# Performance work log

Measured on AMD Instinct MI355X. Metric: run time of the kernel, lower is better.

Reference implementation:

```python
import jax, jax.numpy as jnp
import numpy as np

N, E = 50000, 1600000
C_IN, C_H, C_OUT = 36, 64, 64
EPS = 1e-16  # PyG softmax denominator epsilon


def setup_inputs() -> dict:
    key = jax.random.key(0)
    ks = jax.random.split(key, 48)
    inp = {}
    inp["features"] = jax.random.normal(ks[0], (N, C_IN), dtype=jnp.float32)
    inp["edge_attr"] = jax.random.uniform(ks[1], (E, 1), dtype=jnp.float32)
    inp["edge_index"] = jax.random.randint(ks[2], (2, E), 0, N, dtype=jnp.int32)
    dims = [(C_IN, C_H), (C_H, C_H), (C_H, C_H), (C_H, C_OUT)]
    i = 3
    for l, (din, dout) in enumerate(dims, 1):
        s = 1.0 / np.sqrt(din)
        inp[f"Wl{l}"] = jax.random.normal(ks[i], (din, dout), jnp.float32) * s; i += 1
        inp[f"bl{l}"] = jax.random.normal(ks[i], (dout,), jnp.float32) * 0.02; i += 1
        inp[f"Wr{l}"] = jax.random.normal(ks[i], (din, dout), jnp.float32) * s; i += 1
        inp[f"br{l}"] = jax.random.normal(ks[i], (dout,), jnp.float32) * 0.02; i += 1
        inp[f"We{l}"] = jax.random.normal(ks[i], (1, dout), jnp.float32); i += 1
        inp[f"att{l}"] = jax.random.normal(ks[i], (dout,), jnp.float32) * s; i += 1
        inp[f"bo{l}"] = jax.random.normal(ks[i], (dout,), jnp.float32) * 0.02; i += 1
    mlp = [(C_OUT, C_OUT // 2, "m1"), (C_OUT // 2, C_OUT // 4, "m2"), (C_OUT // 4, 1, "m3")]
    for din, dout, tag in mlp:
        s = 1.0 / np.sqrt(din)
        inp[f"W{tag}"] = jax.random.normal(ks[i], (din, dout), jnp.float32) * s; i += 1
        inp[f"b{tag}"] = jax.random.normal(ks[i], (dout,), jnp.float32) * 0.02; i += 1
    return inp


def gatv2_conv(x, src, dst, edge_attr, Wl, bl, Wr, br, We, att, bo):
    """Single-head GATv2Conv with edge features (PyG semantics)."""
    xl = x @ Wl + bl                      # [N, dout] source transform
    xr = x @ Wr + br                      # [N, dout] target transform
    ea = edge_attr @ We                   # [E, dout]
    e = jax.nn.leaky_relu(xl[src] + xr[dst] + ea, 0.2)  # [E, dout]
    score = e @ att                       # [E]
    # segment softmax over edges sharing a destination node
    m = jax.ops.segment_max(score, dst, num_segments=N)
    a = jnp.exp(score - m[dst])
    denom = jax.ops.segment_sum(a, dst, num_segments=N)
    alpha = a / (denom[dst] + EPS)
    out = jax.ops.segment_sum(xl[src] * alpha[:, None], dst, num_segments=N)
    return out + bo


def reference(features, edge_attr, edge_index,
              Wl1, bl1, Wr1, br1, We1, att1, bo1,
              Wl2, bl2, Wr2, br2, We2, att2, bo2,
              Wl3, bl3, Wr3, br3, We3, att3, bo3,
              Wl4, bl4, Wr4, br4, We4, att4, bo4,
              Wm1, bm1, Wm2, bm2, Wm3, bm3):
    src, dst = edge_index[0], edge_index[1]
    x = jax.nn.relu(gatv2_conv(features, src, dst, edge_attr, Wl1, bl1, Wr1, br1, We1, att1, bo1))
    x = jax.nn.relu(gatv2_conv(x, src, dst, edge_attr, Wl2, bl2, Wr2, br2, We2, att2, bo2))
    x = jax.nn.relu(gatv2_conv(x, src, dst, edge_attr, Wl3, bl3, Wr3, br3, We3, att3, bo3))
    x = jax.nn.relu(gatv2_conv(x, src, dst, edge_attr, Wl4, bl4, Wr4, br4, We4, att4, bo4))
    x = jnp.mean(x, axis=-2)              # graph readout -> [C_OUT]
    x = jax.nn.relu(x @ Wm1 + bm1)
    x = jax.nn.relu(x @ Wm2 + bm2)
    return x @ Wm3 + bm3                  # [1]
```

## Files before the change

kernel.cpp:

```cpp
#include <hip/hip_runtime.h>


__device__ __forceinline__ int rfl(int v) { return __builtin_amdgcn_readfirstlane(v); }

#define NBK_MAX 256
#define BCAP 10240

__global__ void __launch_bounds__(256) k_scatter(
    const int* __restrict__ src, const int* __restrict__ dst,
    const float* __restrict__ ea_in,
    int* __restrict__ bcur, uint2* __restrict__ tmp, int E, int nbk) {
  __shared__ int cnt[NBK_MAX];
  __shared__ int cur[NBK_MAX];
  __shared__ int gbase[NBK_MAX];
  int tid = threadIdx.x;
  if (tid < nbk) { cnt[tid] = 0; cur[tid] = 0; }
  __syncthreads();
  int base = blockIdx.x * 4096 + tid;
  uint2 rec[16];
  #pragma unroll
  for (int k = 0; k < 16; k++) {
    int e = base + k * 256;
    if (e < E) {
      unsigned d = (unsigned)dst[e];
      rec[k] = make_uint2((d << 16) | (unsigned)src[e],
                          (unsigned)__float_as_int(ea_in[e]));
      atomicAdd(&cnt[d >> 8], 1);
    } else {
      rec[k] = make_uint2(0u, 0u);
    }
  }
  __syncthreads();
  if (tid < nbk) {
    int c = cnt[tid];
    gbase[tid] = (c > 0) ? atomicAdd(&bcur[tid * 16], c) : 0;
  }
  __syncthreads();
  #pragma unroll
  for (int k = 0; k < 16; k++) {
    int e = base + k * 256;
    if (e < E) {
      int b = (int)(rec[k].x >> 24);
      int slot = atomicAdd(&cur[b], 1);
      tmp[(size_t)b * BCAP + gbase[b] + slot] = rec[k];
    }
  }
}

__global__ void k_bscan(const int* __restrict__ bcur, int* __restrict__ boffs,
                        int nbk, int E) {
  __shared__ int wsum[4];
  int tid = threadIdx.x, lane = tid & 63, wv = tid >> 6;
  int v = (tid < nbk) ? bcur[tid * 16] : 0;
  int x = v;
  #pragma unroll
  for (int o = 1; o < 64; o <<= 1) {
    int t = __shfl_up(x, o, 64);
    if (lane >= o) x += t;
  }
  if (lane == 63) wsum[wv] = x;
  __syncthreads();
  int wo = 0;
  for (int k = 0; k < 4; k++) if (k < wv) wo += wsum[k];
  if (tid < nbk) boffs[tid] = wo + (x - v);
  if (tid == 0) boffs[nbk] = E;
}

__global__ void __launch_bounds__(256) k_csr(const int* __restrict__ bcur,
                                             const int* __restrict__ boffs,
                                             const uint2* __restrict__ tmp,
                                             int2* __restrict__ pairs,
                                             int* __restrict__ rowptr, int N) {
  __shared__ int cnt[256];
  __shared__ int pref[256];
  __shared__ int cur[256];
  __shared__ int wsum[4];
  int b = blockIdx.x;
  int n0 = b << 8;
  int tid = threadIdx.x, lane = tid & 63, wv = tid >> 6;
  cnt[tid] = 0;
  cur[tid] = 0;
  __syncthreads();
  int cb = bcur[b * 16];
  const uint2* tb = tmp + (size_t)b * BCAP;
  int lo = boffs[b];
  for (int k = tid; k < cb; k += 256)
    atomicAdd(&cnt[(int)(tb[k].x >> 16) - n0], 1);
  __syncthreads();
  int v = cnt[tid];
  int x = v;
  #pragma unroll
  for (int o = 1; o < 64; o <<= 1) {
    int t = __shfl_up(x, o, 64);
    if (lane >= o) x += t;
  }
  if (lane == 63) wsum[wv] = x;
  __syncthreads();
  int wo = 0;
  for (int k = 0; k < 4; k++) if (k < wv) wo += wsum[k];
  int start = lo + wo + (x - v);
  pref[tid] = start;
  int nn = n0 + tid;
  if (nn <= N) rowptr[nn] = start;
  __syncthreads();
  for (int k = tid; k < cb; k += 256) {
    uint2 rec = tb[k];
    int local = (int)(rec.x >> 16) - n0;
    int pos = pref[local] + atomicAdd(&cur[local], 1);
    pairs[pos] = make_int2((int)(rec.x & 0xffffu), (int)rec.y);
  }
}

template <int DIN>
__global__ void __launch_bounds__(256) k_transform(
    const float* __restrict__ x, const float* __restrict__ Wl, const float* __restrict__ bl,
    const float* __restrict__ Wr, const float* __restrict__ br,
    float* __restrict__ xl, float* __restrict__ xr, int nNodes) {
  __shared__ __align__(16) float sWl[DIN * 64];
  __shared__ __align__(16) float sWr[DIN * 64];
  __shared__ float sx[64][DIN + 1];
  int tid = threadIdx.x;
  for (int i = tid; i < DIN * 64; i += 256) { sWl[i] = Wl[i]; sWr[i] = Wr[i]; }
  int nb = blockIdx.x * 64;
  for (int i = tid; i < 64 * DIN; i += 256) {
    int ln = i / DIN, c = i % DIN;
    int g = nb + ln;
    sx[ln][c] = (g < nNodes) ? x[(size_t)g * DIN + c] : 0.f;
  }
  __syncthreads();
  int c4 = (tid & 15) * 4;
  int ns = (tid >> 4) * 4;
  float4 bl4 = *(const float4*)(bl + c4);
  float4 br4 = *(const float4*)(br + c4);
  float4 L0 = bl4, L1 = bl4, L2 = bl4, L3 = bl4;
  float4 R0 = br4, R1 = br4, R2 = br4, R3 = br4;
  const float* x0 = sx[ns + 0];
  const float* x1 = sx[ns + 1];
  const float* x2 = sx[ns + 2];
  const float* x3 = sx[ns + 3];
  #pragma unroll 4
  for (int k = 0; k < DIN; k++) {
    float4 wl = *(const float4*)(sWl + k * 64 + c4);
    float4 wr = *(const float4*)(sWr + k * 64 + c4);
    float a = x0[k], bb = x1[k], c = x2[k], dd = x3[k];
    L0.x = fmaf(a, wl.x, L0.x);  L0.y = fmaf(a, wl.y, L0.y);
    L0.z = fmaf(a, wl.z, L0.z);  L0.w = fmaf(a, wl.w, L0.w);
    R0.x = fmaf(a, wr.x, R0.x);  R0.y = fmaf(a, wr.y, R0.y);
    R0.z = fmaf(a, wr.z, R0.z);  R0.w = fmaf(a, wr.w, R0.w);
    L1.x = fmaf(bb, wl.x, L1.x); L1.y = fmaf(bb, wl.y, L1.y);
    L1.z = fmaf(bb, wl.z, L1.z); L1.w = fmaf(bb, wl.w, L1.w);
    R1.x = fmaf(bb, wr.x, R1.x); R1.y = fmaf(bb, wr.y, R1.y);
    R1.z = fmaf(bb, wr.z, R1.z); R1.w = fmaf(bb, wr.w, R1.w);
    L2.x = fmaf(c, wl.x, L2.x);  L2.y = fmaf(c, wl.y, L2.y);
    L2.z = fmaf(c, wl.z, L2.z);  L2.w = fmaf(c, wl.w, L2.w);
    R2.x = fmaf(c, wr.x, R2.x);  R2.y = fmaf(c, wr.y, R2.y);
    R2.z = fmaf(c, wr.z, R2.z);  R2.w = fmaf(c, wr.w, R2.w);
    L3.x = fmaf(dd, wl.x, L3.x); L3.y = fmaf(dd, wl.y, L3.y);
    L3.z = fmaf(dd, wl.z, L3.z); L3.w = fmaf(dd, wl.w, L3.w);
    R3.x = fmaf(dd, wr.x, R3.x); R3.y = fmaf(dd, wr.y, R3.y);
    R3.z = fmaf(dd, wr.z, R3.z); R3.w = fmaf(dd, wr.w, R3.w);
  }
  int g = nb + ns;
  if (g + 0 < nNodes) { *(float4*)(xl + (size_t)(g+0)*64 + c4) = L0; *(float4*)(xr + (size_t)(g+0)*64 + c4) = R0; }
  if (g + 1 < nNodes) { *(float4*)(xl + (size_t)(g+1)*64 + c4) = L1; *(float4*)(xr + (size_t)(g+1)*64 + c4) = R1; }
  if (g + 2 < nNodes) { *(float4*)(xl + (size_t)(g+2)*64 + c4) = L2; *(float4*)(xr + (size_t)(g+2)*64 + c4) = R2; }
  if (g + 3 < nNodes) { *(float4*)(xl + (size_t)(g+3)*64 + c4) = L3; *(float4*)(xr + (size_t)(g+3)*64 + c4) = R3; }
}

#define SC1(T, EA, OUT) { float u, acc; \
  u = T.x + fmaf(EA, We4.x, xr4.x); u = fmaxf(u, 0.2f * u); acc = at4.x * u; \
  u = T.y + fmaf(EA, We4.y, xr4.y); u = fmaxf(u, 0.2f * u); acc = fmaf(at4.y, u, acc); \
  u = T.z + fmaf(EA, We4.z, xr4.z); u = fmaxf(u, 0.2f * u); acc = fmaf(at4.z, u, acc); \
  u = T.w + fmaf(EA, We4.w, xr4.w); u = fmaxf(u, 0.2f * u); acc = fmaf(at4.w, u, acc); \
  OUT = acc; }

__global__ void __launch_bounds__(256, 5) k_edge(
    const float* __restrict__ xl, const float* __restrict__ xr,
    const int* __restrict__ rowptr, const int2* __restrict__ pairs,
    const float* __restrict__ We, const float* __restrict__ att,
    const float* __restrict__ bo, float* __restrict__ xout, int nNodes) {
  int lane = threadIdx.x & 63;
  int wv = rfl((int)(threadIdx.x >> 6));
  int n = rfl(blockIdx.x * 4 + wv);
  if (n >= nNodes) return;
  int c4 = lane & 15;
  int r  = lane >> 4;
  int cb = c4 * 4;

  float4 We4 = *(const float4*)(We + cb);
  float4 at4 = *(const float4*)(att + cb);
  float4 xr4 = *(const float4*)(xr + (size_t)n * 64 + cb);
  int s0 = rfl(rowptr[n]);
  int s1 = rfl(rowptr[n + 1]);
  int last = s1 - 1;

  float m = -3.0e38f, d = 0.f;
  float4 A = {0.f, 0.f, 0.f, 0.f};

  for (int kb = s0; kb < s1; kb += 16) {
    int cnt = rfl(min(16, s1 - kb));
    int2 p0 = pairs[min(kb + r,      last)];
    int2 p1 = pairs[min(kb + 4 + r,  last)];
    int2 p2 = pairs[min(kb + 8 + r,  last)];
    int2 p3 = pairs[min(kb + 12 + r, last)];
    float ea0 = __int_as_float(p0.y);
    float ea1 = __int_as_float(p1.y);
    float ea2 = __int_as_float(p2.y);
    float ea3 = __int_as_float(p3.y);

    float4 t0 = *(const float4*)(xl + (size_t)(unsigned)p0.x * 64 + cb);
    float4 t1 = *(const float4*)(xl + (size_t)(unsigned)p1.x * 64 + cb);
    float4 t2 = *(const float4*)(xl + (size_t)(unsigned)p2.x * 64 + cb);
    float4 t3 = *(const float4*)(xl + (size_t)(unsigned)p3.x * 64 + cb);

    float sc0, sc1, sc2, sc3;
    SC1(t0, ea0, sc0)
    SC1(t1, ea1, sc1)
    SC1(t2, ea2, sc2)
    SC1(t3, ea3, sc3)

    #pragma unroll
    for (int o = 1; o <= 8; o <<= 1) {
      sc0 += __shfl_xor(sc0, o, 64);
      sc1 += __shfl_xor(sc1, o, 64);
      sc2 += __shfl_xor(sc2, o, 64);
      sc3 += __shfl_xor(sc3, o, 64);
    }
    sc0 = (r < cnt)      ? sc0 : -3.0e38f;
    sc1 = (4 + r < cnt)  ? sc1 : -3.0e38f;
    sc2 = (8 + r < cnt)  ? sc2 : -3.0e38f;
    sc3 = (12 + r < cnt) ? sc3 : -3.0e38f;

    float mc = fmaxf(fmaxf(sc0, sc1), fmaxf(sc2, sc3));
    mc = fmaxf(mc, __shfl_xor(mc, 16, 64));
    mc = fmaxf(mc, __shfl_xor(mc, 32, 64));
    float newm = fmaxf(m, mc);
    float rf = __expf(m - newm);
    float a0 = __expf(sc0 - newm);
    float a1 = __expf(sc1 - newm);
    float a2 = __expf(sc2 - newm);
    float a3 = __expf(sc3 - newm);
    float ds = (a0 + a1) + (a2 + a3);
    ds += __shfl_xor(ds, 16, 64);
    ds += __shfl_xor(ds, 32, 64);
    d = d * rf + ds;
    m = newm;

    A.x = fmaf(a0, t0.x, A.x * rf); A.y = fmaf(a0, t0.y, A.y * rf);
    A.z = fmaf(a0, t0.z, A.z * rf); A.w = fmaf(a0, t0.w, A.w * rf);
    A.x = fmaf(a1, t1.x, A.x); A.y = fmaf(a1, t1.y, A.y);
    A.z = fmaf(a1, t1.z, A.z); A.w = fmaf(a1, t1.w, A.w);
    A.x = fmaf(a2, t2.x, A.x); A.y = fmaf(a2, t2.y, A.y);
    A.z = fmaf(a2, t2.z, A.z); A.w = fmaf(a2, t2.w, A.w);
    A.x = fmaf(a3, t3.x, A.x); A.y = fmaf(a3, t3.y, A.y);
    A.z = fmaf(a3, t3.z, A.z); A.w = fmaf(a3, t3.w, A.w);
  }

  A.x += __shfl_xor(A.x, 16, 64); A.y += __shfl_xor(A.y, 16, 64);
  A.z += __shfl_xor(A.z, 16, 64); A.w += __shfl_xor(A.w, 16, 64);
  A.x += __shfl_xor(A.x, 32, 64); A.y += __shfl_xor(A.y, 32, 64);
  A.z += __shfl_xor(A.z, 32, 64); A.w += __shfl_xor(A.w, 32, 64);

  float inv = 1.f / (d + 1e-16f);
  if (r == 0) {
    float4 bo4 = *(const float4*)(bo + cb);
    float4 o4;
    o4.x = fmaxf(fmaf(A.x, inv, bo4.x), 0.f);
    o4.y = fmaxf(fmaf(A.y, inv, bo4.y), 0.f);
    o4.z = fmaxf(fmaf(A.z, inv, bo4.z), 0.f);
    o4.w = fmaxf(fmaf(A.w, inv, bo4.w), 0.f);
    *(float4*)(xout + (size_t)n * 64 + cb) = o4;
  }
}

__global__ void k_mean(const float* __restrict__ x, double* __restrict__ meanbuf, int nNodes) {
  __shared__ float sacc[256];
  int lane = threadIdx.x & 63;
  int wv = threadIdx.x >> 6;
  int gw = blockIdx.x * 4 + wv;
  int stride = gridDim.x * 4;
  float acc = 0.f;
  for (int n = gw; n < nNodes; n += stride) acc += x[(size_t)n * 64 + lane];
  sacc[threadIdx.x] = acc;
  __syncthreads();
  if (threadIdx.x < 64) {
    float a = sacc[threadIdx.x] + sacc[threadIdx.x + 64] + sacc[threadIdx.x + 128] + sacc[threadIdx.x + 192];
    atomicAdd(&meanbuf[lane], (double)a);
  }
}

__global__ void k_mlp(const double* __restrict__ meanbuf,
                      const float* __restrict__ Wm1, const float* __restrict__ bm1,
                      const float* __restrict__ Wm2, const float* __restrict__ bm2,
                      const float* __restrict__ Wm3, const float* __restrict__ bm3,
                      float* __restrict__ out, double invN) {
  __shared__ float xm[64];
  __shared__ float h1[32];
  __shared__ float h2[16];
  int t = threadIdx.x;
  xm[t] = (float)(meanbuf[t] * invN);
  __syncthreads();
  if (t < 32) {
    float a = bm1[t];
    for (int c = 0; c < 64; c++) a = fmaf(xm[c], Wm1[c * 32 + t], a);
    h1[t] = fmaxf(a, 0.f);
  }
  __syncthreads();
  if (t < 16) {
    float a = bm2[t];
    for (int c = 0; c < 32; c++) a = fmaf(h1[c], Wm2[c * 16 + t], a);
    h2[t] = fmaxf(a, 0.f);
  }
  __syncthreads();
  if (t == 0) {
    float a = bm3[0];
    for (int c = 0; c < 16; c++) a = fmaf(h2[c], Wm3[c], a);
    out[0] = a;
  }
}

extern "C" void kernel_launch(void* const* d_in, const int* in_sizes, int n_in,
                              void* d_out, int out_size, void* d_ws, size_t ws_size,
                              hipStream_t stream) {
  (void)n_in; (void)out_size; (void)ws_size;
  const int N = in_sizes[0] / 36;
  const int E = in_sizes[1];

  const float* feat = (const float*)d_in[0];
  const float* eat  = (const float*)d_in[1];
  const int*   eidx = (const int*)d_in[2];
  const int* src = eidx;
  const int* dst = eidx + E;

  const float* L[4][7];
  for (int l = 0; l < 4; l++)
    for (int j = 0; j < 7; j++) L[l][j] = (const float*)d_in[3 + l * 7 + j];
  const float* Wm1 = (const float*)d_in[31];
  const float* bm1 = (const float*)d_in[32];
  const float* Wm2 = (const float*)d_in[33];
  const float* bm2 = (const float*)d_in[34];
  const float* Wm3 = (const float*)d_in[35];
  const float* bm3 = (const float*)d_in[36];

  const int NBK = (N + 255) >> 8;

  char* ws = (char*)d_ws;
  size_t off = 0;
  auto alloc = [&](size_t bytes) {
    off = (off + 511) & ~(size_t)511;
    void* p = ws + off;
    off += bytes;
    return p;
  };
  int*    bcur    = (int*)alloc((size_t)NBK * 16 * 4);
  double* meanbuf = (double*)alloc(64 * 8);
  size_t zero_bytes = off;
  int*    boffs   = (int*)alloc((size_t)(NBK + 1) * 4);
  int*    rowptr  = (int*)alloc((size_t)(N + 1) * 4);
  int2*   pairs   = (int2*)alloc((size_t)E * 8);
  float*  xA      = (float*)alloc((size_t)N * 64 * 4);
  float*  xB      = (float*)alloc((size_t)N * 64 * 4);
  float*  xC      = (float*)alloc((size_t)N * 64 * 4);
  uint2*  tmp     = (uint2*)xB;

  hipMemsetAsync(d_ws, 0, zero_bytes, stream);

  int sgrid = (E + 4095) / 4096;
  int tgrid = (N + 63) / 64;
  int ngrid = (N + 3) / 4;

  k_scatter<<<sgrid, 256, 0, stream>>>(src, dst, eat, bcur, tmp, E, NBK);
  k_bscan<<<1, 256, 0, stream>>>(bcur, boffs, NBK, E);
  k_csr<<<NBK, 256, 0, stream>>>(bcur, boffs, tmp, pairs, rowptr, N);

  for (int l = 0; l < 4; l++) {
    if (l == 0)
      k_transform<36><<<tgrid, 256, 0, stream>>>(feat, L[0][0], L[0][1], L[0][2], L[0][3], xA, xB, N);
    else
      k_transform<64><<<tgrid, 256, 0, stream>>>(xC, L[l][0], L[l][1], L[l][2], L[l][3], xA, xB, N);
    k_edge<<<ngrid, 256, 0, stream>>>(xA, xB, rowptr, pairs,
                                      L[l][4], L[l][5], L[l][6], xC, N);
  }

  k_mean<<<256, 256, 0, stream>>>(xC, meanbuf, N);
  k_mlp<<<1, 64, 0, stream>>>(meanbuf, Wm1, bm1, Wm2, bm2, Wm3, bm3, (float*)d_out, 1.0 / (double)N);
}
```

Baseline: 497.6 us.

## Fuse edge scatter with layer-1 transform and fold bucket scan into CSR kernel

The edge bucket-scatter and the first layer's node transform now run as one launch, with blocks split by index between the two jobs, so the two independent pieces of work overlap on the GPU. The separate bucket-offset scan kernel is removed. Each CSR block instead sums the preceding bucket counts itself, and the CSR kernel grows to 1024 threads. The scatter block size is halved and the temporary buffer gets its own allocation, aliased with xC, instead of sharing xB, which the transform now writes. This cuts two launches and their serialization, at the cost of redundant prefix sums and a smaller per-bucket capacity (BCAP 9216).

```diff
diff --git a/kernel.cpp b/kernel.cpp
--- a/kernel.cpp
+++ b/kernel.cpp
@@ -4,106 +4,159 @@
 __device__ __forceinline__ int rfl(int v) { return __builtin_amdgcn_readfirstlane(v); }
 
 #define NBK_MAX 256
-#define BCAP 10240
-
-__global__ void __launch_bounds__(256) k_scatter(
+#define BCAP 9216
+
+__global__ void __launch_bounds__(256) k_build1(
     const int* __restrict__ src, const int* __restrict__ dst,
-    const float* __restrict__ ea_in,
-    int* __restrict__ bcur, uint2* __restrict__ tmp, int E, int nbk) {
-  __shared__ int cnt[NBK_MAX];
-  __shared__ int cur[NBK_MAX];
-  __shared__ int gbase[NBK_MAX];
+    const float* __restrict__ ea_in, int* __restrict__ bcur,
+    uint2* __restrict__ tmp, int E, int nbk, int SG,
+    const float* __restrict__ x, const float* __restrict__ Wl,
+    const float* __restrict__ bl, const float* __restrict__ Wr,
+    const float* __restrict__ br, float* __restrict__ xl,
+    float* __restrict__ xr, int nNodes) {
+  __shared__ __align__(16) float smem[6976];
   int tid = threadIdx.x;
-  if (tid < nbk) { cnt[tid] = 0; cur[tid] = 0; }
-  __syncthreads();
-  int base = blockIdx.x * 4096 + tid;
-  uint2 rec[16];
-  #pragma unroll
-  for (int k = 0; k < 16; k++) {
-    int e = base + k * 256;
-    if (e < E) {
-      unsigned d = (unsigned)dst[e];
-      rec[k] = make_uint2((d << 16) | (unsigned)src[e],
-                          (unsigned)__float_as_int(ea_in[e]));
-      atomicAdd(&cnt[d >> 8], 1);
-    } else {
-      rec[k] = make_uint2(0u, 0u);
-    }
-  }
-  __syncthreads();
-  if (tid < nbk) {
-    int c = cnt[tid];
-    gbase[tid] = (c > 0) ? atomicAdd(&bcur[tid * 16], c) : 0;
-  }
-  __syncthreads();
-  #pragma unroll
-  for (int k = 0; k < 16; k++) {
-    int e = base + k * 256;
-    if (e < E) {
-      int b = (int)(rec[k].x >> 24);
-      int slot = atomicAdd(&cur[b], 1);
-      tmp[(size_t)b * BCAP + gbase[b] + slot] = rec[k];
-    }
-  }
-}
-
-__global__ void k_bscan(const int* __restrict__ bcur, int* __restrict__ boffs,
-                        int nbk, int E) {
-  __shared__ int wsum[4];
-  int tid = threadIdx.x, lane = tid & 63, wv = tid >> 6;
-  int v = (tid < nbk) ? bcur[tid * 16] : 0;
-  int x = v;
-  #pragma unroll
-  for (int o = 1; o < 64; o <<= 1) {
-    int t = __shfl_up(x, o, 64);
-    if (lane >= o) x += t;
-  }
-  if (lane == 63) wsum[wv] = x;
-  __syncthreads();
-  int wo = 0;
-  for (int k = 0; k < 4; k++) if (k < wv) wo += wsum[k];
-  if (tid < nbk) boffs[tid] = wo + (x - v);
-  if (tid == 0) boffs[nbk] = E;
-}
-
-__global__ void __launch_bounds__(256) k_csr(const int* __restrict__ bcur,
-                                             const int* __restrict__ boffs,
-                                             const uint2* __restrict__ tmp,
-                                             int2* __restrict__ pairs,
-                                             int* __restrict__ rowptr, int N) {
+  if ((int)blockIdx.x < SG) {
+    int* cnt = (int*)smem;
+    int* cur = cnt + 256;
+    int* gb  = cur + 256;
+    if (tid < nbk) { cnt[tid] = 0; cur[tid] = 0; }
+    __syncthreads();
+    int base = blockIdx.x * 2048 + tid;
+    uint2 rec[8];
+    #pragma unroll
+    for (int k = 0; k < 8; k++) {
+      int e = base + k * 256;
+      if (e < E) {
+        unsigned d = (unsigned)dst[e];
+        rec[k] = make_uint2((d << 16) | (unsigned)src[e],
+                            (unsigned)__float_as_int(ea_in[e]));
+        atomicAdd(&cnt[d >> 8], 1);
+      } else {
+        rec[k] = make_uint2(0u, 0u);
+      }
+    }
+    __syncthreads();
+    if (tid < nbk) {
+      int c = cnt[tid];
+      gb[tid] = (c > 0) ? atomicAdd(&bcur[tid * 16], c) : 0;
+    }
+    __syncthreads();
+    #pragma unroll
+    for (int k = 0; k < 8; k++) {
+      int e = base + k * 256;
+      if (e < E) {
+        int b = (int)(rec[k].x >> 24);
+        int slot = atomicAdd(&cur[b], 1);
+        tmp[(size_t)b * BCAP + gb[b] + slot] = rec[k];
+      }
+    }
+  } else {
+    const int DIN = 36;
+    float* sWl = smem;
+    float* sWr = smem + 2304;
+    float (*sx)[DIN + 1] = (float(*)[DIN + 1])(smem + 4608);
+    for (int i = tid; i < DIN * 64; i += 256) { sWl[i] = Wl[i]; sWr[i] = Wr[i]; }
+    int nb = ((int)blockIdx.x - SG) * 64;
+    for (int i = tid; i < 64 * DIN; i += 256) {
+      int ln = i / DIN, c = i % DIN;
+      int g = nb + ln;
+      sx[ln][c] = (g < nNodes) ? x[(size_t)g * DIN + c] : 0.f;
+    }
+    __syncthreads();
+    int c4 = (tid & 15) * 4;
+    int ns = (tid >> 4) * 4;
+    float4 bl4 = *(const float4*)(bl + c4);
+    float4 br4 = *(const float4*)(br + c4);
+    float4 L0 = bl4, L1 = bl4, L2 = bl4, L3 = bl4;
+    float4 R0 = br4, R1 = br4, R2 = br4, R3 = br4;
+    const float* x0 = sx[ns + 0];
+    const float* x1 = sx[ns + 1];
+    const float* x2 = sx[ns + 2];
+    const float* x3 = sx[ns + 3];
+    #pragma unroll 4
+    for (int k = 0; k < DIN; k++) {
+      float4 wl = *(const float4*)(sWl + k * 64 + c4);
+      float4 wr = *(const float4*)(sWr + k * 64 + c4);
+      float a = x0[k], bb = x1[k], c = x2[k], dd = x3[k];
+      L0.x = fmaf(a, wl.x, L0.x);  L0.y = fmaf(a, wl.y, L0.y);
+      L0.z = fmaf(a, wl.z, L0.z);  L0.w = fmaf(a, wl.w, L0.w);
+      R0.x = fmaf(a, wr.x, R0.x);  R0.y = fmaf(a, wr.y, R0.y);
+      R0.z = fmaf(a, wr.z, R0.z);  R0.w = fmaf(a, wr.w, R0.w);
+      L1.x = fmaf(bb, wl.x, L1.x); L1.y = fmaf(bb, wl.y, L1.y);
+      L1.z = fmaf(bb, wl.z, L1.z); L1.w = fmaf(bb, wl.w, L1.w);
+      R1.x = fmaf(bb, wr.x, R1.x); R1.y = fmaf(bb, wr.y, R1.y);
+      R1.z = fmaf(bb, wr.z, R1.z); R1.w = fmaf(bb, wr.w, R1.w);
+      L2.x = fmaf(c, wl.x, L2.x);  L2.y = fmaf(c, wl.y, L2.y);
+      L2.z = fmaf(c, wl.z, L2.z);  L2.w = fmaf(c, wl.w, L2.w);
+      R2.x = fmaf(c, wr.x, R2.x);  R2.y = fmaf(c, wr.y, R2.y);
+      R2.z = fmaf(c, wr.z, R2.z);  R2.w = fmaf(c, wr.w, R2.w);
+      L3.x = fmaf(dd, wl.x, L3.x); L3.y = fmaf(dd, wl.y, L3.y);
+      L3.z = fmaf(dd, wl.z, L3.z); L3.w = fmaf(dd, wl.w, L3.w);
+      R3.x = fmaf(dd, wr.x, R3.x); R3.y = fmaf(dd, wr.y, R3.y);
+      R3.z = fmaf(dd, wr.z, R3.z); R3.w = fmaf(dd, wr.w, R3.w);
+    }
+    int g = nb + ns;
+    if (g + 0 < nNodes) { *(float4*)(xl + (size_t)(g+0)*64 + c4) = L0; *(float4*)(xr + (size_t)(g+0)*64 + c4) = R0; }
+    if (g + 1 < nNodes) { *(float4*)(xl + (size_t)(g+1)*64 + c4) = L1; *(float4*)(xr + (size_t)(g+1)*64 + c4) = R1; }
+    if (g + 2 < nNodes) { *(float4*)(xl + (size_t)(g+2)*64 + c4) = L2; *(float4*)(xr + (size_t)(g+2)*64 + c4) = R2; }
+    if (g + 3 < nNodes) { *(float4*)(xl + (size_t)(g+3)*64 + c4) = L3; *(float4*)(xr + (size_t)(g+3)*64 + c4) = R3; }
+  }
+}
+
+__global__ void __launch_bounds__(1024) k_csr(const int* __restrict__ bcur,
+                                              const uint2* __restrict__ tmp,
+                                              int2* __restrict__ pairs,
+                                              int* __restrict__ rowptr,
+                                              int N, int nbk) {
   __shared__ int cnt[256];
   __shared__ int pref[256];
   __shared__ int cur[256];
-  __shared__ int wsum[4];
+  __shared__ int wsum[16];
+  __shared__ int lo_s;
   int b = blockIdx.x;
   int n0 = b << 8;
   int tid = threadIdx.x, lane = tid & 63, wv = tid >> 6;
-  cnt[tid] = 0;
-  cur[tid] = 0;
-  __syncthreads();
+  if (tid < 256) { cnt[tid] = 0; cur[tid] = 0; }
+  int contrib = (tid < nbk && tid < b) ? bcur[tid * 16] : 0;
+  #pragma unroll
+  for (int o = 32; o > 0; o >>= 1) contrib += __shfl_xor(contrib, o, 64);
+  if (lane == 0) wsum[wv] = contrib;
+  __syncthreads();
+  if (tid == 0) {
+    int s = 0;
+    for (int i = 0; i < 16; i++) s += wsum[i];
+    lo_s = s;
+  }
+  __syncthreads();
+  int lo = lo_s;
   int cb = bcur[b * 16];
   const uint2* tb = tmp + (size_t)b * BCAP;
-  int lo = boffs[b];
-  for (int k = tid; k < cb; k += 256)
+  for (int k = tid; k < cb; k += 1024)
     atomicAdd(&cnt[(int)(tb[k].x >> 16) - n0], 1);
   __syncthreads();
-  int v = cnt[tid];
-  int x = v;
-  #pragma unroll
-  for (int o = 1; o < 64; o <<= 1) {
-    int t = __shfl_up(x, o, 64);
-    if (lane >= o) x += t;
-  }
-  if (lane == 63) wsum[wv] = x;
-  __syncthreads();
-  int wo = 0;
-  for (int k = 0; k < 4; k++) if (k < wv) wo += wsum[k];
-  int start = lo + wo + (x - v);
-  pref[tid] = start;
-  int nn = n0 + tid;
-  if (nn <= N) rowptr[nn] = start;
-  __syncthreads();
-  for (int k = tid; k < cb; k += 256) {
+  int v = 0, x = 0;
+  if (tid < 256) {
+    v = cnt[tid];
+    x = v;
+    #pragma unroll
+    for (int o = 1; o < 64; o <<= 1) {
+      int t = __shfl_up(x, o, 64);
+      if (lane >= o) x += t;
+    }
+    if (lane == 63) wsum[wv] = x;
+  }
+  __syncthreads();
+  if (tid < 256) {
+    int wo = 0;
+    for (int k = 0; k < 4; k++) if (k < wv) wo += wsum[k];
+    int start = lo + wo + (x - v);
+    pref[tid] = start;
+    int nn = n0 + tid;
+    if (nn <= N) rowptr[nn] = start;
+  }
+  __syncthreads();
+  for (int k = tid; k < cb; k += 1024) {
     uint2 rec = tb[k];
     int local = (int)(rec.x >> 16) - n0;
     int pos = pref[local] + atomicAdd(&cur[local], 1);
@@ -355,29 +408,29 @@
   int*    bcur    = (int*)alloc((size_t)NBK * 16 * 4);
   double* meanbuf = (double*)alloc(64 * 8);
   size_t zero_bytes = off;
-  int*    boffs   = (int*)alloc((size_t)(NBK + 1) * 4);
   int*    rowptr  = (int*)alloc((size_t)(N + 1) * 4);
   int2*   pairs   = (int2*)alloc((size_t)E * 8);
   float*  xA      = (float*)alloc((size_t)N * 64 * 4);
   float*  xB      = (float*)alloc((size_t)N * 64 * 4);
-  float*  xC      = (float*)alloc((size_t)N * 64 * 4);
-  uint2*  tmp     = (uint2*)xB;
+  uint2*  tmp     = (uint2*)alloc((size_t)NBK * BCAP * 8);
+  float*  xC      = (float*)tmp;
 
   hipMemsetAsync(d_ws, 0, zero_bytes, stream);
 
-  int sgrid = (E + 4095) / 4096;
-  int tgrid = (N + 63) / 64;
+  int SG = (E + 2047) / 2048;
+  int TG = (N + 63) / 64;
+  int tgrid = TG;
   int ngrid = (N + 3) / 4;
 
-  k_scatter<<<sgrid, 256, 0, stream>>>(src, dst, eat, bcur, tmp, E, NBK);
-  k_bscan<<<1, 256, 0, stream>>>(bcur, boffs, NBK, E);
-  k_csr<<<NBK, 256, 0, stream>>>(bcur, boffs, tmp, pairs, rowptr, N);
-
-  for (int l = 0; l < 4; l++) {
-    if (l == 0)
-      k_transform<36><<<tgrid, 256, 0, stream>>>(feat, L[0][0], L[0][1], L[0][2], L[0][3], xA, xB, N);
-    else
-      k_transform<64><<<tgrid, 256, 0, stream>>>(xC, L[l][0], L[l][1], L[l][2], L[l][3], xA, xB, N);
+  k_build1<<<SG + TG, 256, 0, stream>>>(src, dst, eat, bcur, tmp, E, NBK, SG,
+                                        feat, L[0][0], L[0][1], L[0][2], L[0][3],
+                                        xA, xB, N);
+  k_csr<<<NBK, 1024, 0, stream>>>(bcur, tmp, pairs, rowptr, N, NBK);
+  k_edge<<<ngrid, 256, 0, stream>>>(xA, xB, rowptr, pairs,
+                                    L[0][4], L[0][5], L[0][6], xC, N);
+
+  for (int l = 1; l < 4; l++) {
+    k_transform<64><<<tgrid, 256, 0, stream>>>(xC, L[l][0], L[l][1], L[l][2], L[l][3], xA, xB, N);
     k_edge<<<ngrid, 256, 0, stream>>>(xA, xB, rowptr, pairs,
                                       L[l][4], L[l][5], L[l][6], xC, N);
   }
```

Measured after the change: 490.8 us. No clear change (-1.4%).
